# Kernel optimization log

Measured on AMD Instinct MI355X. Metric: run time of the kernel, lower is better.

Reference implementation:

```python
import jax, jax.numpy as jnp
import numpy as np

A = 32        # num_agents (nodes per graph block)
B = 128       # batch graphs
N = B * A     # nodes per timestep = 4096
T = 5         # temporal_window_size
K = 16        # num_belief_states
AD = 8        # action_dim
H = 4         # num_attn_heads
DH = 64       # hidden_dim (per GAT head)
D = H * DH    # feature_dim = 256
HD = D // H   # temporal MHA head dim = 64
L = 64        # latent_dim
FIN = K + AD  # discrete node feature dim = 24


def _block_edges():
    # fully connected within each batch block, incl. self loops (PyG GATConv default)
    s = np.repeat(np.arange(A), A)
    d = np.tile(np.arange(A), A)
    off = (np.arange(B) * A)[:, None]
    src = (off + s[None, :]).reshape(-1)
    dst = (off + d[None, :]).reshape(-1)
    return jnp.asarray(np.stack([src, dst]), dtype=jnp.int32)  # [2, B*A*A]


def setup_inputs():
    key = jax.random.key(0)
    ks = jax.random.split(key, 16)
    g = lambda i, shape, s=0.05: jax.random.normal(ks[i], shape, dtype=jnp.float32) * s
    z = lambda shape: jnp.zeros(shape, jnp.float32)
    return {
        'node_feats': g(0, (T, N, FIN), 1.0),
        'edge_index': _block_edges(),
        'gat1_w': g(1, (FIN, D)), 'gat1_asrc': g(2, (H, DH)), 'gat1_adst': g(3, (H, DH)), 'gat1_b': z((D,)),
        'gat2_w': g(4, (D, D)), 'gat2_asrc': g(5, (H, DH)), 'gat2_adst': g(6, (H, DH)), 'gat2_b': z((D,)),
        'wq': g(7, (D, D)), 'bq': z((D,)),
        'wk': g(8, (D, D)), 'bk': z((D,)),
        'wv': g(9, (D, D)), 'bv': z((D,)),
        'wo': g(10, (D, D)), 'bo': z((D,)),
        'lm_w': g(11, (D, L)), 'lm_b': z((L,)),
        'lv_w': g(12, (D, L)), 'lv_b': z((L,)),
        'ap_w': g(13, (L, AD * A)), 'ap_b': z((AD * A,)),
        'bh_w': g(14, (D, K)), 'bh_b': z((K,)),
    }


def _gat_layer(x, W, a_src, a_dst, b, src, dst):
    # PyG GATConv: per-edge additive attention, softmax over incoming edges of dst
    h = (x @ W).reshape(N, H, DH)
    al_s = (h * a_src[None]).sum(-1)                      # [N,H]
    al_d = (h * a_dst[None]).sum(-1)                      # [N,H]
    e = jax.nn.leaky_relu(al_s[src] + al_d[dst], 0.2)     # [E,H]
    m = jax.ops.segment_max(e, dst, num_segments=N)
    p = jnp.exp(e - m[dst])
    zden = jax.ops.segment_sum(p, dst, num_segments=N)
    alpha = p / (zden[dst] + 1e-16)                       # [E,H]
    out = jax.ops.segment_sum(h[src] * alpha[:, :, None], dst, num_segments=N)
    return out.reshape(N, D) + b


def reference(node_feats, edge_index, gat1_w, gat1_asrc, gat1_adst, gat1_b,
              gat2_w, gat2_asrc, gat2_adst, gat2_b,
              wq, bq, wk, bk, wv, bv, wo, bo,
              lm_w, lm_b, lv_w, lv_b, ap_w, ap_b, bh_w, bh_b):
    src, dst = edge_index[0], edge_index[1]

    def gnn(x):  # two GATConv layers + ReLU (dropout inactive at inference)
        x = jax.nn.relu(_gat_layer(x, gat1_w, gat1_asrc, gat1_adst, gat1_b, src, dst))
        x = jax.nn.relu(_gat_layer(x, gat2_w, gat2_asrc, gat2_adst, gat2_b, src, dst))
        return x

    feats = jax.vmap(gnn)(node_feats)          # [T,N,D]
    ego = feats[:, ::A, :]                     # ego node of each block -> [T,B,D]
    seq = jnp.transpose(ego, (1, 0, 2))        # [B,T,D]

    # temporal MultiheadAttention with causal mask (batch_first)
    q = (seq @ wq + bq).reshape(B, T, H, HD)
    k = (seq @ wk + bk).reshape(B, T, H, HD)
    v = (seq @ wv + bv).reshape(B, T, H, HD)
    scores = jnp.einsum('bthd,bshd->bhts', q, k) / jnp.sqrt(jnp.float32(HD))
    causal = jnp.tril(jnp.ones((T, T), bool))
    scores = jnp.where(causal[None, None], scores, jnp.float32(-1e9))
    attn = jax.nn.softmax(scores, axis=-1)
    ctx = jnp.einsum('bhts,bshd->bthd', attn, v).reshape(B, T, D)
    feat = (ctx @ wo + bo)[:, -1]              # last timestep features [B,D]

    mu = feat @ lm_w + lm_b                    # latent_mean
    logvar = feat @ lv_w + lv_b                # latent_logvar
    act = mu @ ap_w + ap_b                     # action_predictor(latent)
    belief = feat @ bh_w + bh_b                # belief_head(features)
    return jnp.concatenate([mu, logvar, act, belief], axis=-1)  # [B, 2L+AD*A+K]
```

## Files before the change

kernel.cpp:

```cpp
#include <hip/hip_runtime.h>

typedef unsigned short u16;
typedef unsigned int u32;
typedef short bf16x8 __attribute__((ext_vector_type(8)));
typedef float f32x4  __attribute__((ext_vector_type(4)));


__device__ __forceinline__ u16 f2b(float f) {
    unsigned u = __float_as_uint(f);
    return (u16)((u + 0x7FFFu + ((u >> 16) & 1u)) >> 16);
}
__device__ __forceinline__ float b2f(u16 u) {
    return __uint_as_float(((unsigned)u) << 16);
}

__global__ __launch_bounds__(256) void prep_w2_kernel(
    const float* __restrict__ w, u16* __restrict__ wt)
{
    __shared__ float tile[32][33];
    const int bi = blockIdx.x >> 3, bj = blockIdx.x & 7;
    const int r0 = bi * 32, c0 = bj * 32;
    const int lr = threadIdx.x >> 5, lc = threadIdx.x & 31;
    for (int i = lr; i < 32; i += 8)
        tile[i][lc] = w[(r0 + i) * 256 + c0 + lc];
    __syncthreads();
    for (int i = lr; i < 32; i += 8)
        wt[(c0 + i) * 256 + r0 + lc] = f2b(tile[lc][i]);
}

__global__ __launch_bounds__(256, 2) void gat12_kernel(
    const float* __restrict__ x,
    const float* __restrict__ w1, const float* __restrict__ a1s,
    const float* __restrict__ a1d, const float* __restrict__ b1,
    const u16* __restrict__ w2t, const float* __restrict__ a2s,
    const float* __restrict__ a2d, const float* __restrict__ b2,
    u16* __restrict__ ego,
    const float* __restrict__ wq, const float* __restrict__ wk,
    const float* __restrict__ wv, u16* __restrict__ wqkvt)
{
    constexpr int FIN = 24;
    constexpr int HP = 40;
    constexpr int XP = 264;

    __shared__ u16 h1T[256 * HP];
    __shared__ u16 x2s[32 * XP];
    __shared__ u16 alphaT[4 * 32 * HP];
    __shared__ u16 h2s[32 * XP];
    __shared__ float als2[256], ald2[256];
    __shared__ float a1sf[256], a1df[256], a2sf[256], a2df[256];
    __shared__ float b1f[256], b2f_[256];
    __shared__ float alpha0[4][32];

    const int tid = threadIdx.x;

    if (blockIdx.x >= 640) {
        const int bid = blockIdx.x - 640;
        const int m = bid >> 6, tl = bid & 63;
        const float* src = (m == 0) ? wq : (m == 1) ? wk : wv;
        u16* dst = wqkvt + m * 65536;
        float (*tile)[33] = (float(*)[33])h1T;
        const int bi = tl >> 3, bj = tl & 7;
        const int r0 = bi * 32, c0 = bj * 32;
        const int lr = tid >> 5, lc = tid & 31;
        for (int i = lr; i < 32; i += 8)
            tile[i][lc] = src[(r0 + i) * 256 + c0 + lc];
        __syncthreads();
        for (int i = lr; i < 32; i += 8)
            dst[(c0 + i) * 256 + r0 + lc] = f2b(tile[lc][i]);
        return;
    }

    const int wave = tid >> 6;
    const int l    = tid & 63;
    const int l15  = l & 15;
    const int quad = l >> 4;
    const int t    = blockIdx.x >> 7;
    const int b    = blockIdx.x & 127;
    const long row0 = (long)(t * 4096 + b * 32);

    float* xst = (float*)alphaT;
    if (tid < 192) {
        const float4 v = *(const float4*)(x + row0 * FIN + tid * 4);
        const int r = tid / 6, c = (tid % 6) * 4;
        *(float4*)&xst[r * 28 + c] = v;
    }
    a1sf[tid] = a1s[tid];  a1df[tid] = a1d[tid];
    a2sf[tid] = a2s[tid];  a2df[tid] = a2d[tid];
    b1f[tid]  = b1[tid];   b2f_[tid]  = b2[tid];
    __syncthreads();

    {
        float acc[32];
#pragma unroll
        for (int i = 0; i < 32; ++i) acc[i] = 0.f;
        for (int k0 = 0; k0 < FIN; k0 += 4) {
            const float w0 = w1[(k0 + 0) * 256 + tid];
            const float wA = w1[(k0 + 1) * 256 + tid];
            const float wB = w1[(k0 + 2) * 256 + tid];
            const float wC = w1[(k0 + 3) * 256 + tid];
#pragma unroll
            for (int i = 0; i < 32; ++i) {
                const float4 xv = *(const float4*)&xst[i * 28 + k0];
                acc[i] += xv.x * w0 + xv.y * wA + xv.z * wB + xv.w * wC;
            }
        }
        __syncthreads();
        u32 pk[16];
#pragma unroll
        for (int s = 0; s < 16; ++s)
            pk[s] = (u32)f2b(acc[2 * s]) | ((u32)f2b(acc[2 * s + 1]) << 16);
        u32* dst = (u32*)&h1T[tid * HP];
#pragma unroll
        for (int s = 0; s < 4; ++s)
            *(uint4*)&dst[s * 4] = make_uint4(pk[4*s], pk[4*s+1], pk[4*s+2], pk[4*s+3]);
    }
    __syncthreads();

    {
        const int pair = tid >> 7;
        const int id = tid & 127;
        const int i = id >> 2, hh = id & 3;
        float as = 0.f, ad = 0.f;
        for (int cc = 0; cc < 32; ++cc) {
            const int c = (((cc + tid) & 31) | (pair << 5)) + hh * 64;
            const float hv = b2f(h1T[c * HP + i]);
            as += hv * a1sf[c];
            ad += hv * a1df[c];
        }
        als2[tid] = as;
        ald2[tid] = ad;
    }
    __syncthreads();

    if (tid < 128) {
        const int hh = tid & 3, dd = tid >> 2;
        const float advv = ald2[tid] + ald2[128 + tid];
        float e[32]; float m = -1e30f;
#pragma unroll
        for (int s = 0; s < 32; ++s) {
            float v = (als2[s * 4 + hh] + als2[128 + s * 4 + hh]) + advv;
            v = v > 0.f ? v : 0.2f * v;
            e[s] = v; m = fmaxf(m, v);
        }
        float sum = 0.f;
#pragma unroll
        for (int s = 0; s < 32; ++s) { float p = __expf(e[s] - m); e[s] = p; sum += p; }
        const float inv = 1.f / (sum + 1e-16f);
        u32 pk[16];
#pragma unroll
        for (int s = 0; s < 16; ++s)
            pk[s] = (u32)f2b(e[2*s] * inv) | ((u32)f2b(e[2*s+1] * inv) << 16);
        u32* dst = (u32*)&alphaT[(hh * 32 + dd) * HP];
#pragma unroll
        for (int s = 0; s < 4; ++s)
            *(uint4*)&dst[s * 4] = make_uint4(pk[4*s], pk[4*s+1], pk[4*s+2], pk[4*s+3]);
    }
    __syncthreads();

    {
        const int hh = wave;
        bf16x8 af[2];
#pragma unroll
        for (int mt = 0; mt < 2; ++mt)
            af[mt] = *(const bf16x8*)&alphaT[(hh * 32 + mt * 16 + l15) * HP + quad * 8];
        f32x4 acc[2][4];
#pragma unroll
        for (int mt = 0; mt < 2; ++mt)
#pragma unroll
            for (int nt = 0; nt < 4; ++nt) acc[mt][nt] = (f32x4){0.f, 0.f, 0.f, 0.f};
#pragma unroll
        for (int nt = 0; nt < 4; ++nt) {
            const bf16x8 bf = *(const bf16x8*)&h1T[(hh * 64 + nt * 16 + l15) * HP + quad * 8];
            acc[0][nt] = __builtin_amdgcn_mfma_f32_16x16x32_bf16(af[0], bf, acc[0][nt], 0, 0, 0);
            acc[1][nt] = __builtin_amdgcn_mfma_f32_16x16x32_bf16(af[1], bf, acc[1][nt], 0, 0, 0);
        }
#pragma unroll
        for (int mt = 0; mt < 2; ++mt)
#pragma unroll
            for (int nt = 0; nt < 4; ++nt) {
                const int col = hh * 64 + nt * 16 + l15;
                const float bb = b1f[col];
#pragma unroll
                for (int r = 0; r < 4; ++r) {
                    const int d = mt * 16 + quad * 4 + r;
                    x2s[d * XP + col] = f2b(fmaxf(acc[mt][nt][r] + bb, 0.f));
                }
            }
    }
    __syncthreads();

    {
        const int n0 = wave * 64;
        f32x4 acc[2][4];
#pragma unroll
        for (int mt = 0; mt < 2; ++mt)
#pragma unroll
            for (int nt = 0; nt < 4; ++nt) acc[mt][nt] = (f32x4){0.f, 0.f, 0.f, 0.f};
        for (int k0 = 0; k0 < 256; k0 += 32) {
            const int kb = k0 + quad * 8;
            const bf16x8 a0 = *(const bf16x8*)&x2s[(l15)      * XP + kb];
            const bf16x8 a1 = *(const bf16x8*)&x2s[(16 + l15) * XP + kb];
#pragma unroll
            for (int nt = 0; nt < 4; ++nt) {
                const bf16x8 bb = *(const bf16x8*)(w2t + (n0 + nt * 16 + l15) * 256 + kb);
                acc[0][nt] = __builtin_amdgcn_mfma_f32_16x16x32_bf16(a0, bb, acc[0][nt], 0, 0, 0);
                acc[1][nt] = __builtin_amdgcn_mfma_f32_16x16x32_bf16(a1, bb, acc[1][nt], 0, 0, 0);
            }
        }
#pragma unroll
        for (int mt = 0; mt < 2; ++mt)
#pragma unroll
            for (int nt = 0; nt < 4; ++nt)
#pragma unroll
                for (int r = 0; r < 4; ++r)
                    h2s[(mt * 16 + quad * 4 + r) * XP + n0 + nt * 16 + l15] =
                        f2b(acc[mt][nt][r]);
    }
    __syncthreads();

    {
        const int pair = tid >> 7;
        const int id = tid & 127;
        const int i = id >> 2, hh = id & 3;
        float as = 0.f, ad = 0.f;
        for (int cc = 0; cc < 32; ++cc) {
            const int c = (((cc + tid) & 31) | (pair << 5)) + hh * 64;
            const float hv = b2f(h2s[i * XP + c]);
            as += hv * a2sf[c];
            ad += hv * a2df[c];
        }
        als2[tid] = as;
        ald2[tid] = ad;
    }
    __syncthreads();

    if (tid < 4) {
        const int hh = tid;
        const float advv = ald2[hh] + ald2[128 + hh];
        float e[32]; float m = -1e30f;
#pragma unroll
        for (int s = 0; s < 32; ++s) {
            float v = (als2[s * 4 + hh] + als2[128 + s * 4 + hh]) + advv;
            v = v > 0.f ? v : 0.2f * v;
            e[s] = v; m = fmaxf(m, v);
        }
        float sum = 0.f;
#pragma unroll
        for (int s = 0; s < 32; ++s) { float p = __expf(e[s] - m); e[s] = p; sum += p; }
        const float inv = 1.f / (sum + 1e-16f);
#pragma unroll
        for (int s = 0; s < 32; ++s) alpha0[hh][s] = e[s] * inv;
    }
    __syncthreads();

    {
        const int hh = tid >> 6;
        float a = 0.f;
#pragma unroll
        for (int s = 0; s < 32; ++s)
            a += alpha0[hh][s] * b2f(h2s[s * XP + tid]);
        ego[((long)(t * 128 + b)) * 256 + tid] = f2b(fmaxf(a + b2f_[tid], 0.f));
    }
}

__global__ __launch_bounds__(256) void qkv_kernel(
    const u16* __restrict__ ego, const u16* __restrict__ wqkvt,
    const float* __restrict__ bq, const float* __restrict__ bk,
    const float* __restrict__ bv_, float* __restrict__ qkv)
{
    const int tid  = threadIdx.x;
    const int wave = tid >> 6;
    const int l    = tid & 63;
    const int l15  = l & 15;
    const int quad = l >> 4;
    const int gx = blockIdx.x % 20;
    const int gy = blockIdx.x / 20;
    const int r0 = gx * 32;
    const int n0 = wave * 64;
    const u16* wsrc = wqkvt + gy * 65536;
    const float* bias = (gy == 0) ? bq : (gy == 1) ? bk : bv_;

    f32x4 acc[2][4];
#pragma unroll
    for (int mt = 0; mt < 2; ++mt)
#pragma unroll
        for (int nt = 0; nt < 4; ++nt) acc[mt][nt] = (f32x4){0.f, 0.f, 0.f, 0.f};

    for (int k0 = 0; k0 < 256; k0 += 32) {
        const int kb = k0 + quad * 8;
        const bf16x8 a0 = *(const bf16x8*)(ego + (r0 + l15)      * 256 + kb);
        const bf16x8 a1 = *(const bf16x8*)(ego + (r0 + 16 + l15) * 256 + kb);
#pragma unroll
        for (int nt = 0; nt < 4; ++nt) {
            const bf16x8 bb = *(const bf16x8*)(wsrc + (n0 + nt * 16 + l15) * 256 + kb);
            acc[0][nt] = __builtin_amdgcn_mfma_f32_16x16x32_bf16(a0, bb, acc[0][nt], 0, 0, 0);
            acc[1][nt] = __builtin_amdgcn_mfma_f32_16x16x32_bf16(a1, bb, acc[1][nt], 0, 0, 0);
        }
    }
#pragma unroll
    for (int mt = 0; mt < 2; ++mt)
#pragma unroll
        for (int nt = 0; nt < 4; ++nt)
#pragma unroll
            for (int r = 0; r < 4; ++r) {
                const int row = r0 + mt * 16 + quad * 4 + r;
                const int col = n0 + nt * 16 + l15;
                qkv[(long)row * 768 + gy * 256 + col] = acc[mt][nt][r] + bias[col];
            }
}

__global__ __launch_bounds__(256) void attn_tail_kernel(
    const float* __restrict__ qkv,
    const float* __restrict__ wo, const float* __restrict__ bo,
    const float* __restrict__ lm_w, const float* __restrict__ lm_b,
    const float* __restrict__ lv_w, const float* __restrict__ lv_b,
    const float* __restrict__ ap_w, const float* __restrict__ ap_b,
    const float* __restrict__ bh_w, const float* __restrict__ bh_b,
    float* __restrict__ out)
{
    __shared__ float q4[256], kk[5 * 256], vv[5 * 256];
    __shared__ float ctx[256], feat[256], mu[64];
    __shared__ float scl[20], attw[20];

    const int j = threadIdx.x;
    const int b = blockIdx.x;

    q4[j] = qkv[(long)(512 + b) * 768 + j];
#pragma unroll
    for (int t = 0; t < 5; ++t) {
        const long r = (long)(t * 128 + b) * 768;
        kk[t * 256 + j] = qkv[r + 256 + j];
        vv[t * 256 + j] = qkv[r + 512 + j];
    }
    __syncthreads();

    if (j < 20) {
        const int hh = j / 5, ss = j % 5;
        float sc = 0.f;
        for (int c = 0; c < 64; ++c)
            sc += q4[hh * 64 + c] * kk[ss * 256 + hh * 64 + c];
        scl[j] = sc * 0.125f;
    }
    __syncthreads();

    if (j < 4) {
        float m = -1e30f;
        for (int ss = 0; ss < 5; ++ss) m = fmaxf(m, scl[j * 5 + ss]);
        float p[5], sum = 0.f;
        for (int ss = 0; ss < 5; ++ss) { p[ss] = __expf(scl[j * 5 + ss] - m); sum += p[ss]; }
        for (int ss = 0; ss < 5; ++ss) attw[j * 5 + ss] = p[ss] / sum;
    }
    __syncthreads();

    {
        const int hh = j >> 6;
        float c = 0.f;
#pragma unroll
        for (int ss = 0; ss < 5; ++ss) c += attw[hh * 5 + ss] * vv[ss * 256 + j];
        ctx[j] = c;
    }
    __syncthreads();

    {
        float a0 = 0.f, a1 = 0.f, a2 = 0.f, a3 = 0.f;
#pragma unroll 2
        for (int i = 0; i < 256; i += 4) {
            a0 += ctx[i + 0] * wo[(i + 0) * 256 + j];
            a1 += ctx[i + 1] * wo[(i + 1) * 256 + j];
            a2 += ctx[i + 2] * wo[(i + 2) * 256 + j];
            a3 += ctx[i + 3] * wo[(i + 3) * 256 + j];
        }
        feat[j] = bo[j] + ((a0 + a1) + (a2 + a3));
    }
    __syncthreads();

    float* ob = out + b * 400;
    if (j < 64) {
        float a0 = 0.f, a1 = 0.f, a2 = 0.f, a3 = 0.f;
#pragma unroll 2
        for (int i = 0; i < 256; i += 4) {
            a0 += feat[i + 0] * lm_w[(i + 0) * 64 + j];
            a1 += feat[i + 1] * lm_w[(i + 1) * 64 + j];
            a2 += feat[i + 2] * lm_w[(i + 2) * 64 + j];
            a3 += feat[i + 3] * lm_w[(i + 3) * 64 + j];
        }
        const float m = lm_b[j] + ((a0 + a1) + (a2 + a3));
        mu[j] = m;
        ob[j] = m;
    } else if (j < 128) {
        const int c = j - 64;
        float a0 = 0.f, a1 = 0.f, a2 = 0.f, a3 = 0.f;
#pragma unroll 2
        for (int i = 0; i < 256; i += 4) {
            a0 += feat[i + 0] * lv_w[(i + 0) * 64 + c];
            a1 += feat[i + 1] * lv_w[(i + 1) * 64 + c];
            a2 += feat[i + 2] * lv_w[(i + 2) * 64 + c];
            a3 += feat[i + 3] * lv_w[(i + 3) * 64 + c];
        }
        ob[64 + c] = lv_b[c] + ((a0 + a1) + (a2 + a3));
    } else if (j < 144) {
        const int c = j - 128;
        float a0 = 0.f, a1 = 0.f, a2 = 0.f, a3 = 0.f;
#pragma unroll 2
        for (int i = 0; i < 256; i += 4) {
            a0 += feat[i + 0] * bh_w[(i + 0) * 16 + c];
            a1 += feat[i + 1] * bh_w[(i + 1) * 16 + c];
            a2 += feat[i + 2] * bh_w[(i + 2) * 16 + c];
            a3 += feat[i + 3] * bh_w[(i + 3) * 16 + c];
        }
        ob[384 + c] = bh_b[c] + ((a0 + a1) + (a2 + a3));
    }
    __syncthreads();

    {
        float a0 = 0.f, a1 = 0.f, a2 = 0.f, a3 = 0.f;
#pragma unroll
        for (int i = 0; i < 64; i += 4) {
            a0 += mu[i + 0] * ap_w[(i + 0) * 256 + j];
            a1 += mu[i + 1] * ap_w[(i + 1) * 256 + j];
            a2 += mu[i + 2] * ap_w[(i + 2) * 256 + j];
            a3 += mu[i + 3] * ap_w[(i + 3) * 256 + j];
        }
        ob[128 + j] = ap_b[j] + ((a0 + a1) + (a2 + a3));
    }
}

extern "C" void kernel_launch(void* const* d_in, const int* in_sizes, int n_in,
                              void* d_out, int out_size, void* d_ws, size_t ws_size,
                              hipStream_t stream)
{
    const float* node_feats = (const float*)d_in[0];
    const float* g1w  = (const float*)d_in[2];
    const float* g1as = (const float*)d_in[3];
    const float* g1ad = (const float*)d_in[4];
    const float* g1b  = (const float*)d_in[5];
    const float* g2w  = (const float*)d_in[6];
    const float* g2as = (const float*)d_in[7];
    const float* g2ad = (const float*)d_in[8];
    const float* g2b  = (const float*)d_in[9];
    const float* wq = (const float*)d_in[10]; const float* bq = (const float*)d_in[11];
    const float* wk = (const float*)d_in[12]; const float* bk = (const float*)d_in[13];
    const float* wv = (const float*)d_in[14]; const float* bv = (const float*)d_in[15];
    const float* wo = (const float*)d_in[16]; const float* bo = (const float*)d_in[17];
    const float* lm_w = (const float*)d_in[18]; const float* lm_b = (const float*)d_in[19];
    const float* lv_w = (const float*)d_in[20]; const float* lv_b = (const float*)d_in[21];
    const float* ap_w = (const float*)d_in[22]; const float* ap_b = (const float*)d_in[23];
    const float* bh_w = (const float*)d_in[24]; const float* bh_b = (const float*)d_in[25];

    char* ws = (char*)d_ws;
    u16*   ego   = (u16*)ws;
    u16*   w2t   = (u16*)(ws + 327680);
    u16*   wqkvt = (u16*)(ws + 458752);
    float* qkv   = (float*)(ws + 851968);

    prep_w2_kernel<<<64, 256, 0, stream>>>(g2w, w2t);
    gat12_kernel<<<832, 256, 0, stream>>>(node_feats, g1w, g1as, g1ad, g1b,
                                          w2t, g2as, g2ad, g2b, ego,
                                          wq, wk, wv, wqkvt);
    qkv_kernel<<<60, 256, 0, stream>>>(ego, wqkvt, bq, bk, bv, qkv);
    attn_tail_kernel<<<128, 256, 0, stream>>>(qkv, wo, bo, lm_w, lm_b, lv_w, lv_b,
                                              ap_w, ap_b, bh_w, bh_b, (float*)d_out);
}
```

Baseline: 169.4 us.

## Batch output projection and heads as MFMA GEMMs, trim GAT LDS for occupancy

```diff
diff --git a/kernel.cpp b/kernel.cpp
--- a/kernel.cpp
+++ b/kernel.cpp
@@ -28,7 +28,7 @@
         wt[(c0 + i) * 256 + r0 + lc] = f2b(tile[lc][i]);
 }
 
-__global__ __launch_bounds__(256, 2) void gat12_kernel(
+__global__ __launch_bounds__(256, 3) void gat12_kernel(
     const float* __restrict__ x,
     const float* __restrict__ w1, const float* __restrict__ a1s,
     const float* __restrict__ a1d, const float* __restrict__ b1,
@@ -36,7 +36,11 @@
     const float* __restrict__ a2d, const float* __restrict__ b2,
     u16* __restrict__ ego,
     const float* __restrict__ wq, const float* __restrict__ wk,
-    const float* __restrict__ wv, u16* __restrict__ wqkvt)
+    const float* __restrict__ wv, const float* __restrict__ wo,
+    const float* __restrict__ lm_w, const float* __restrict__ lv_w,
+    const float* __restrict__ bh_w, const float* __restrict__ ap_w,
+    u16* __restrict__ wqkvt, u16* __restrict__ wot,
+    u16* __restrict__ headT, u16* __restrict__ apT)
 {
     constexpr int FIN = 24;
     constexpr int HP = 40;
@@ -45,28 +49,45 @@
     __shared__ u16 h1T[256 * HP];
     __shared__ u16 x2s[32 * XP];
     __shared__ u16 alphaT[4 * 32 * HP];
-    __shared__ u16 h2s[32 * XP];
     __shared__ float als2[256], ald2[256];
     __shared__ float a1sf[256], a1df[256], a2sf[256], a2df[256];
-    __shared__ float b1f[256], b2f_[256];
     __shared__ float alpha0[4][32];
 
     const int tid = threadIdx.x;
 
     if (blockIdx.x >= 640) {
         const int bid = blockIdx.x - 640;
-        const int m = bid >> 6, tl = bid & 63;
-        const float* src = (m == 0) ? wq : (m == 1) ? wk : wv;
-        u16* dst = wqkvt + m * 65536;
+        const float* src; u16* dst;
+        int C = 256, S = 256, roff = 0, bi, bj;
+        if (bid < 192) {
+            const int m = bid >> 6, tl = bid & 63;
+            src = (m == 0) ? wq : (m == 1) ? wk : wv;
+            dst = wqkvt + m * 65536;
+            bi = tl >> 3; bj = tl & 7;
+        } else if (bid < 256) {
+            const int tl = bid - 192;
+            src = wo; dst = wot; bi = tl >> 3; bj = tl & 7;
+        } else if (bid < 272) {
+            const int tl = bid - 256;
+            src = lm_w; dst = headT; C = 64; bi = tl >> 1; bj = tl & 1;
+        } else if (bid < 288) {
+            const int tl = bid - 272;
+            src = lv_w; dst = headT; C = 64; roff = 64; bi = tl >> 1; bj = tl & 1;
+        } else if (bid < 296) {
+            src = bh_w; dst = headT; C = 16; roff = 128; bi = bid - 288; bj = 0;
+        } else {
+            const int tl = bid - 296;
+            src = ap_w; dst = apT; S = 64; bi = tl >> 3; bj = tl & 7;
+        }
         float (*tile)[33] = (float(*)[33])h1T;
-        const int bi = tl >> 3, bj = tl & 7;
         const int r0 = bi * 32, c0 = bj * 32;
         const int lr = tid >> 5, lc = tid & 31;
+        const int cw = (C - c0 < 32) ? (C - c0) : 32;
         for (int i = lr; i < 32; i += 8)
-            tile[i][lc] = src[(r0 + i) * 256 + c0 + lc];
+            if (lc < cw) tile[i][lc] = src[(r0 + i) * C + c0 + lc];
         __syncthreads();
-        for (int i = lr; i < 32; i += 8)
-            dst[(c0 + i) * 256 + r0 + lc] = f2b(tile[lc][i]);
+        for (int i = lr; i < cw; i += 8)
+            dst[(roff + c0 + i) * S + r0 + lc] = f2b(tile[lc][i]);
         return;
     }
 
@@ -86,7 +107,6 @@
     }
     a1sf[tid] = a1s[tid];  a1df[tid] = a1d[tid];
     a2sf[tid] = a2s[tid];  a2df[tid] = a2d[tid];
-    b1f[tid]  = b1[tid];   b2f_[tid]  = b2[tid];
     __syncthreads();
 
     {
@@ -179,7 +199,7 @@
 #pragma unroll
             for (int nt = 0; nt < 4; ++nt) {
                 const int col = hh * 64 + nt * 16 + l15;
-                const float bb = b1f[col];
+                const float bb = b1[col];
 #pragma unroll
                 for (int r = 0; r < 4; ++r) {
                     const int d = mt * 16 + quad * 4 + r;
@@ -189,6 +209,7 @@
     }
     __syncthreads();
 
+    u16* h2s = h1T;
     {
         const int n0 = wave * 64;
         f32x4 acc[2][4];
@@ -207,6 +228,7 @@
                 acc[1][nt] = __builtin_amdgcn_mfma_f32_16x16x32_bf16(a1, bb, acc[1][nt], 0, 0, 0);
             }
         }
+        __syncthreads();
 #pragma unroll
         for (int mt = 0; mt < 2; ++mt)
 #pragma unroll
@@ -259,7 +281,7 @@
 #pragma unroll
         for (int s = 0; s < 32; ++s)
             a += alpha0[hh][s] * b2f(h2s[s * XP + tid]);
-        ego[((long)(t * 128 + b)) * 256 + tid] = f2b(fmaxf(a + b2f_[tid], 0.f));
+        ego[((long)(t * 128 + b)) * 256 + tid] = f2b(fmaxf(a + b2[tid], 0.f));
     }
 }
 
@@ -273,8 +295,10 @@
     const int l    = tid & 63;
     const int l15  = l & 15;
     const int quad = l >> 4;
-    const int gx = blockIdx.x % 20;
-    const int gy = blockIdx.x / 20;
+    int gx, gy;
+    if (blockIdx.x < 20)      { gy = 1; gx = blockIdx.x; }
+    else if (blockIdx.x < 40) { gy = 2; gx = blockIdx.x - 20; }
+    else                      { gy = 0; gx = 16 + (blockIdx.x - 40); }
     const int r0 = gx * 32;
     const int n0 = wave * 64;
     const u16* wsrc = wqkvt + gy * 65536;
@@ -309,17 +333,10 @@
             }
 }
 
-__global__ __launch_bounds__(256) void attn_tail_kernel(
-    const float* __restrict__ qkv,
-    const float* __restrict__ wo, const float* __restrict__ bo,
-    const float* __restrict__ lm_w, const float* __restrict__ lm_b,
-    const float* __restrict__ lv_w, const float* __restrict__ lv_b,
-    const float* __restrict__ ap_w, const float* __restrict__ ap_b,
-    const float* __restrict__ bh_w, const float* __restrict__ bh_b,
-    float* __restrict__ out)
+__global__ __launch_bounds__(256) void attn_kernel(
+    const float* __restrict__ qkv, u16* __restrict__ ctx_g)
 {
     __shared__ float q4[256], kk[5 * 256], vv[5 * 256];
-    __shared__ float ctx[256], feat[256], mu[64];
     __shared__ float scl[20], attw[20];
 
     const int j = threadIdx.x;
@@ -357,71 +374,122 @@
         float c = 0.f;
 #pragma unroll
         for (int ss = 0; ss < 5; ++ss) c += attw[hh * 5 + ss] * vv[ss * 256 + j];
-        ctx[j] = c;
-    }
-    __syncthreads();
-
-    {
-        float a0 = 0.f, a1 = 0.f, a2 = 0.f, a3 = 0.f;
-#pragma unroll 2
-        for (int i = 0; i < 256; i += 4) {
-            a0 += ctx[i + 0] * wo[(i + 0) * 256 + j];
-            a1 += ctx[i + 1] * wo[(i + 1) * 256 + j];
-            a2 += ctx[i + 2] * wo[(i + 2) * 256 + j];
-            a3 += ctx[i + 3] * wo[(i + 3) * 256 + j];
-        }
-        feat[j] = bo[j] + ((a0 + a1) + (a2 + a3));
-    }
-    __syncthreads();
-
-    float* ob = out + b * 400;
-    if (j < 64) {
-        float a0 = 0.f, a1 = 0.f, a2 = 0.f, a3 = 0.f;
-#pragma unroll 2
-        for (int i = 0; i < 256; i += 4) {
-            a0 += feat[i + 0] * lm_w[(i + 0) * 64 + j];
-            a1 += feat[i + 1] * lm_w[(i + 1) * 64 + j];
-            a2 += feat[i + 2] * lm_w[(i + 2) * 64 + j];
-            a3 += feat[i + 3] * lm_w[(i + 3) * 64 + j];
-        }
-        const float m = lm_b[j] + ((a0 + a1) + (a2 + a3));
-        mu[j] = m;
-        ob[j] = m;
-    } else if (j < 128) {
-        const int c = j - 64;
-        float a0 = 0.f, a1 = 0.f, a2 = 0.f, a3 = 0.f;
-#pragma unroll 2
-        for (int i = 0; i < 256; i += 4) {
-            a0 += feat[i + 0] * lv_w[(i + 0) * 64 + c];
-            a1 += feat[i + 1] * lv_w[(i + 1) * 64 + c];
-            a2 += feat[i + 2] * lv_w[(i + 2) * 64 + c];
-            a3 += feat[i + 3] * lv_w[(i + 3) * 64 + c];
-        }
-        ob[64 + c] = lv_b[c] + ((a0 + a1) + (a2 + a3));
-    } else if (j < 144) {
-        const int c = j - 128;
-        float a0 = 0.f, a1 = 0.f, a2 = 0.f, a3 = 0.f;
-#pragma unroll 2
-        for (int i = 0; i < 256; i += 4) {
-            a0 += feat[i + 0] * bh_w[(i + 0) * 16 + c];
-            a1 += feat[i + 1] * bh_w[(i + 1) * 16 + c];
-            a2 += feat[i + 2] * bh_w[(i + 2) * 16 + c];
-            a3 += feat[i + 3] * bh_w[(i + 3) * 16 + c];
-        }
-        ob[384 + c] = bh_b[c] + ((a0 + a1) + (a2 + a3));
-    }
-    __syncthreads();
-
-    {
-        float a0 = 0.f, a1 = 0.f, a2 = 0.f, a3 = 0.f;
-#pragma unroll
-        for (int i = 0; i < 64; i += 4) {
-            a0 += mu[i + 0] * ap_w[(i + 0) * 256 + j];
-            a1 += mu[i + 1] * ap_w[(i + 1) * 256 + j];
-            a2 += mu[i + 2] * ap_w[(i + 2) * 256 + j];
-            a3 += mu[i + 3] * ap_w[(i + 3) * 256 + j];
-        }
-        ob[128 + j] = ap_b[j] + ((a0 + a1) + (a2 + a3));
+        ctx_g[b * 256 + j] = f2b(c);
+    }
+}
+
+__global__ __launch_bounds__(256) void tail_kernel(
+    const u16* __restrict__ ctx_g, const u16* __restrict__ wot,
+    const u16* __restrict__ headT, const u16* __restrict__ apT,
+    const float* __restrict__ bo,
+    const float* __restrict__ lm_b, const float* __restrict__ lv_b,
+    const float* __restrict__ bh_b, const float* __restrict__ ap_b,
+    float* __restrict__ out)
+{
+    constexpr int FP = 264;
+    constexpr int MP = 72;
+    __shared__ u16 fs[32 * FP];
+    __shared__ u16 mus[32 * MP];
+
+    const int tid  = threadIdx.x;
+    const int wave = tid >> 6;
+    const int l    = tid & 63;
+    const int l15  = l & 15;
+    const int quad = l >> 4;
+    const int r0   = blockIdx.x * 32;
+
+    {
+        const int n0 = wave * 64;
+        f32x4 acc[2][4];
+#pragma unroll
+        for (int mt = 0; mt < 2; ++mt)
+#pragma unroll
+            for (int nt = 0; nt < 4; ++nt) acc[mt][nt] = (f32x4){0.f, 0.f, 0.f, 0.f};
+        for (int k0 = 0; k0 < 256; k0 += 32) {
+            const int kb = k0 + quad * 8;
+            const bf16x8 a0 = *(const bf16x8*)(ctx_g + (r0 + l15)      * 256 + kb);
+            const bf16x8 a1 = *(const bf16x8*)(ctx_g + (r0 + 16 + l15) * 256 + kb);
+#pragma unroll
+            for (int nt = 0; nt < 4; ++nt) {
+                const bf16x8 bb = *(const bf16x8*)(wot + (n0 + nt * 16 + l15) * 256 + kb);
+                acc[0][nt] = __builtin_amdgcn_mfma_f32_16x16x32_bf16(a0, bb, acc[0][nt], 0, 0, 0);
+                acc[1][nt] = __builtin_amdgcn_mfma_f32_16x16x32_bf16(a1, bb, acc[1][nt], 0, 0, 0);
+            }
+        }
+#pragma unroll
+        for (int mt = 0; mt < 2; ++mt)
+#pragma unroll
+            for (int nt = 0; nt < 4; ++nt) {
+                const int col = n0 + nt * 16 + l15;
+                const float bb = bo[col];
+#pragma unroll
+                for (int r = 0; r < 4; ++r)
+                    fs[(mt * 16 + quad * 4 + r) * FP + col] = f2b(acc[mt][nt][r] + bb);
+            }
+    }
+    __syncthreads();
+
+    for (int nt = wave; nt < 9; nt += 4) {
+        const int n0 = nt * 16;
+        f32x4 acc[2];
+        acc[0] = (f32x4){0.f, 0.f, 0.f, 0.f};
+        acc[1] = (f32x4){0.f, 0.f, 0.f, 0.f};
+        for (int k0 = 0; k0 < 256; k0 += 32) {
+            const int kb = k0 + quad * 8;
+            const bf16x8 a0 = *(const bf16x8*)&fs[(l15)      * FP + kb];
+            const bf16x8 a1 = *(const bf16x8*)&fs[(16 + l15) * FP + kb];
+            const bf16x8 bb = *(const bf16x8*)(headT + (n0 + l15) * 256 + kb);
+            acc[0] = __builtin_amdgcn_mfma_f32_16x16x32_bf16(a0, bb, acc[0], 0, 0, 0);
+            acc[1] = __builtin_amdgcn_mfma_f32_16x16x32_bf16(a1, bb, acc[1], 0, 0, 0);
+        }
+        const int col = n0 + l15;
+#pragma unroll
+        for (int mt = 0; mt < 2; ++mt)
+#pragma unroll
+            for (int r = 0; r < 4; ++r) {
+                const int row = mt * 16 + quad * 4 + r;
+                float v = acc[mt][r];
+                if (col < 64) {
+                    v += lm_b[col];
+                    out[(long)(r0 + row) * 400 + col] = v;
+                    mus[row * MP + col] = f2b(v);
+                } else if (col < 128) {
+                    v += lv_b[col - 64];
+                    out[(long)(r0 + row) * 400 + col] = v;
+                } else {
+                    v += bh_b[col - 128];
+                    out[(long)(r0 + row) * 400 + 256 + col] = v;
+                }
+            }
+    }
+    __syncthreads();
+
+    {
+#pragma unroll
+        for (int i = 0; i < 4; ++i) {
+            const int n0 = (wave * 4 + i) * 16;
+            f32x4 acc[2];
+            acc[0] = (f32x4){0.f, 0.f, 0.f, 0.f};
+            acc[1] = (f32x4){0.f, 0.f, 0.f, 0.f};
+#pragma unroll
+            for (int k0 = 0; k0 < 64; k0 += 32) {
+                const int kb = k0 + quad * 8;
+                const bf16x8 a0 = *(const bf16x8*)&mus[(l15)      * MP + kb];
+                const bf16x8 a1 = *(const bf16x8*)&mus[(16 + l15) * MP + kb];
+                const bf16x8 bb = *(const bf16x8*)(apT + (n0 + l15) * 64 + kb);
+                acc[0] = __builtin_amdgcn_mfma_f32_16x16x32_bf16(a0, bb, acc[0], 0, 0, 0);
+                acc[1] = __builtin_amdgcn_mfma_f32_16x16x32_bf16(a1, bb, acc[1], 0, 0, 0);
+            }
+            const int col = n0 + l15;
+            const float bb = ap_b[col];
+#pragma unroll
+            for (int mt = 0; mt < 2; ++mt)
+#pragma unroll
+                for (int r = 0; r < 4; ++r) {
+                    const int row = mt * 16 + quad * 4 + r;
+                    out[(long)(r0 + row) * 400 + 128 + col] = acc[mt][r] + bb;
+                }
+        }
     }
 }
 
@@ -452,12 +520,18 @@
     u16*   w2t   = (u16*)(ws + 327680);
     u16*   wqkvt = (u16*)(ws + 458752);
     float* qkv   = (float*)(ws + 851968);
+    u16*   wot   = (u16*)(ws + 2818048);
+    u16*   headT = (u16*)(ws + 2949120);
+    u16*   apT   = (u16*)(ws + 3022848);
+    u16*   ctx_g = (u16*)(ws + 3055616);
 
     prep_w2_kernel<<<64, 256, 0, stream>>>(g2w, w2t);
-    gat12_kernel<<<832, 256, 0, stream>>>(node_feats, g1w, g1as, g1ad, g1b,
+    gat12_kernel<<<952, 256, 0, stream>>>(node_feats, g1w, g1as, g1ad, g1b,
                                           w2t, g2as, g2ad, g2b, ego,
-                                          wq, wk, wv, wqkvt);
-    qkv_kernel<<<60, 256, 0, stream>>>(ego, wqkvt, bq, bk, bv, qkv);
-    attn_tail_kernel<<<128, 256, 0, stream>>>(qkv, wo, bo, lm_w, lm_b, lv_w, lv_b,
-                                              ap_w, ap_b, bh_w, bh_b, (float*)d_out);
-}
+                                          wq, wk, wv, wo, lm_w, lv_w, bh_w, ap_w,
+                                          wqkvt, wot, headT, apT);
+    qkv_kernel<<<44, 256, 0, stream>>>(ego, wqkvt, bq, bk, bv, qkv);
+    attn_kernel<<<128, 256, 0, stream>>>(qkv, ctx_g);
+    tail_kernel<<<4, 256, 0, stream>>>(ctx_g, wot, headT, apT, bo,
+                                       lm_b, lv_b, bh_b, ap_b, (float*)d_out);
+}
```

Measured after the change: 164.1 us. -3.1%, faster.
